# Optimization experiments

Measured on AMD Instinct MI355X. Metric: run time of the kernel, lower is better.

Reference implementation:

```python
import jax, jax.numpy as jnp
import numpy as np

EPS = 1e-5

def _ln(x, g, b):
    m = jnp.mean(x, -1, keepdims=True)
    v = jnp.var(x, -1, keepdims=True)
    return (x - m) / jnp.sqrt(v + EPS) * g + b

def _rel_shift(x):
    # x: [B, qlen, klen, n_head] -- TransformerXL relative shift
    b, q, k, n = x.shape
    xp = jnp.pad(x, ((0, 0), (0, 0), (1, 0), (0, 0)))  # zero-pad along klen front
    xp = xp.reshape(b, k + 1, q, n)[:, 1:]
    return xp.reshape(b, q, k, n)

def setup_inputs() -> dict:
    key = jax.random.key(0)
    B, Q, D, N, DH, DI = 4, 1024, 1024, 16, 64, 4096
    ks = jax.random.split(key, 9)
    s = 0.02
    w = jax.random.normal(ks[0], (B, Q, D), jnp.float32)
    r = jax.random.normal(ks[1], (1, Q, D), jnp.float32)
    attention_mask = jnp.triu(jnp.ones((Q, Q), bool), k=1)  # 1 == masked (causal)
    qkv_w = jax.random.normal(ks[2], (3 * D, D), jnp.float32) * s
    r_w = jax.random.normal(ks[3], (D, D), jnp.float32) * s
    o_w = jax.random.normal(ks[4], (D, D), jnp.float32) * s
    r_w_bias = jax.random.normal(ks[5], (N, DH), jnp.float32) * s
    r_r_bias = jax.random.normal(ks[6], (N, DH), jnp.float32) * s
    ln1_g = jnp.ones(D, jnp.float32); ln1_b = jnp.zeros(D, jnp.float32)
    ff_w1 = jax.random.normal(ks[7], (DI, D), jnp.float32) * s
    ff_b1 = jnp.zeros(DI, jnp.float32)
    ff_w2 = jax.random.normal(ks[8], (D, DI), jnp.float32) * s
    ff_b2 = jnp.zeros(D, jnp.float32)
    ln2_g = jnp.ones(D, jnp.float32); ln2_b = jnp.zeros(D, jnp.float32)
    return dict(w=w, r=r, attention_mask=attention_mask, qkv_w=qkv_w, r_w=r_w,
                o_w=o_w, r_w_bias=r_w_bias, r_r_bias=r_r_bias, ln1_g=ln1_g,
                ln1_b=ln1_b, ff_w1=ff_w1, ff_b1=ff_b1, ff_w2=ff_w2, ff_b2=ff_b2,
                ln2_g=ln2_g, ln2_b=ln2_b)

def reference(w, r, attention_mask, qkv_w, r_w, o_w, r_w_bias, r_r_bias,
              ln1_g, ln1_b, ff_w1, ff_b1, ff_w2, ff_b2, ln2_g, ln2_b):
    B, Q, D = w.shape
    N, DH = r_w_bias.shape
    # QKV projection (post-lnorm path, no mem)
    heads = w @ qkv_w.T  # [B,Q,3D]
    q, k, v = jnp.split(heads, 3, axis=-1)
    q = q.reshape(B, Q, N, DH)
    k = k.reshape(B, Q, N, DH)
    v = v.reshape(B, Q, N, DH)
    rk = (r[0] @ r_w.T).reshape(Q, N, DH)  # [rlen,N,DH]
    # content (AC) and position (BD) terms, computed in fp32 as in original
    AC = jnp.einsum('bind,bjnd->bijn', q + r_w_bias, k)
    BD = _rel_shift(jnp.einsum('bind,jnd->bijn', q + r_r_bias, rk))
    score = (AC + BD) * (1.0 / jnp.sqrt(jnp.float32(DH)))
    score = jnp.where(attention_mask[None, :, :, None], -1e30, score)
    prob = jax.nn.softmax(score, axis=2)  # softmax over klen
    av = jnp.einsum('bijn,bjnd->bind', prob, v).reshape(B, Q, D)
    out1 = _ln(w + av @ o_w.T, ln1_g, ln1_b)  # deepnorm_alpha = 1.0
    ff = jax.nn.relu(out1 @ ff_w1.T + ff_b1) @ ff_w2.T + ff_b2
    return _ln(out1 + ff, ln2_g, ln2_b)
```

## Files before the change

kernel.cpp:

```cpp
#include <hip/hip_runtime.h>
#include <hip/hip_bf16.h>

typedef __attribute__((ext_vector_type(8))) short short8;
typedef __attribute__((ext_vector_type(4))) short short4v;
typedef __attribute__((ext_vector_type(4))) float floatx4;

__device__ inline float bs2f(short s) {
    unsigned int u = ((unsigned int)(unsigned short)s) << 16;
    float f; __builtin_memcpy(&f, &u, 4); return f;
}
__device__ inline short f2bs(float f) {
    __hip_bfloat16 h = __float2bfloat16(f);
    unsigned short u; __builtin_memcpy(&u, &h, 2); return (short)u;
}
__device__ inline float ldf(const float* p)           { return *p; }
__device__ inline float ldf(const __hip_bfloat16* p)  { return __bfloat162float(*p); }
__device__ inline void  stf(float* p, float v)          { *p = v; }
__device__ inline void  stf(__hip_bfloat16* p, float v) { *p = __float2bfloat16(v); }

__device__ inline void gl_lds16(const short* g, short* l) {
    __builtin_amdgcn_global_load_lds(
        (const __attribute__((address_space(1))) void*)g,
        (__attribute__((address_space(3))) void*)l, 16, 0, 0);
}

__global__ __launch_bounds__(256) void f2b_all_kernel(
    const float* __restrict__ s0, const float* __restrict__ s1,
    const float* __restrict__ s2, const float* __restrict__ s3,
    const float* __restrict__ s4, const float* __restrict__ s5,
    const float* __restrict__ s6, __hip_bfloat16* __restrict__ dst)
{
    const long id  = blockIdx.x;
    const long gid = id * 1024 + threadIdx.x * 4;
    const float* src; long base;
    if      (id < 4096)  { src = s0; base = 0; }
    else if (id < 5120)  { src = s1; base = 4096L  * 1024; }
    else if (id < 8192)  { src = s2; base = 5120L  * 1024; }
    else if (id < 9216)  { src = s3; base = 8192L  * 1024; }
    else if (id < 10240) { src = s4; base = 9216L  * 1024; }
    else if (id < 14336) { src = s5; base = 10240L * 1024; }
    else                 { src = s6; base = 14336L * 1024; }
    const float4 v = *(const float4*)(src + (gid - base));
    dst[gid + 0] = __float2bfloat16(v.x);
    dst[gid + 1] = __float2bfloat16(v.y);
    dst[gid + 2] = __float2bfloat16(v.z);
    dst[gid + 3] = __float2bfloat16(v.w);
}

__global__ __launch_bounds__(256, 2) void gemm128_nt_kernel(
    const __hip_bfloat16* __restrict__ A,
    const __hip_bfloat16* __restrict__ Bw,
    __hip_bfloat16* __restrict__ C,
    int M, int N, int K,
    const float* __restrict__ bias,
    int do_relu)
{
    __shared__ short lA[128 * 32];
    __shared__ short lB[128 * 32];

    const int lane = threadIdx.x & 63;
    const int w    = threadIdx.x >> 6;
    const int m16  = lane & 15;
    const int quad = lane >> 4;
    const int wr   = w >> 1, wc = w & 1;

    const long i0 = (long)blockIdx.y * 128;
    const long j0 = (long)blockIdx.x * 128;

    const short* Ap = (const short*)A;
    const short* Bp = (const short*)Bw;

    floatx4 acc[4][4];
    #pragma unroll
    for (int a = 0; a < 4; ++a)
        #pragma unroll
        for (int b = 0; b < 4; ++b) acc[a][b] = (floatx4){0.f, 0.f, 0.f, 0.f};

    const int srow = w * 32 + (lane >> 2);
    const int scol = (lane & 3) * 8;
    const short* ga = Ap + (i0 + srow) * K + scol;
    const short* gb = Bp + (j0 + srow) * K + scol;
    short* la = lA + (w * 32) * 32;
    short* lb = lB + (w * 32) * 32;

    for (int k0 = 0; k0 < K; k0 += 32) {
        __syncthreads();
        gl_lds16(ga + k0,            la);
        gl_lds16(ga + 16 * K + k0,   la + 16 * 32);
        gl_lds16(gb + k0,            lb);
        gl_lds16(gb + 16 * K + k0,   lb + 16 * 32);
        __syncthreads();

        short8 af[4], bf[4];
        #pragma unroll
        for (int rb = 0; rb < 4; ++rb)
            af[rb] = *(const short8*)&lA[(wr * 64 + rb * 16 + m16) * 32 + quad * 8];
        #pragma unroll
        for (int cb = 0; cb < 4; ++cb)
            bf[cb] = *(const short8*)&lB[(wc * 64 + cb * 16 + m16) * 32 + quad * 8];
        #pragma unroll
        for (int rb = 0; rb < 4; ++rb)
            #pragma unroll
            for (int cb = 0; cb < 4; ++cb)
                acc[rb][cb] = __builtin_amdgcn_mfma_f32_16x16x32_bf16(
                    af[rb], bf[cb], acc[rb][cb], 0, 0, 0);
    }

    #pragma unroll
    for (int cb = 0; cb < 4; ++cb) {
        const long j = j0 + wc * 64 + cb * 16 + m16;
        const float bv = bias ? bias[j] : 0.f;
        #pragma unroll
        for (int rb = 0; rb < 4; ++rb) {
            #pragma unroll
            for (int rr = 0; rr < 4; ++rr) {
                const long row = i0 + wr * 64 + rb * 16 + quad * 4 + rr;
                float v = acc[rb][cb][rr] + bv;
                if (do_relu) v = fmaxf(v, 0.f);
                C[row * N + j] = __float2bfloat16(v);
            }
        }
    }
}

__global__ __launch_bounds__(256, 2) void gemm128_splitk_kernel(
    const __hip_bfloat16* __restrict__ A,
    const __hip_bfloat16* __restrict__ Bw,
    __hip_bfloat16* __restrict__ C0,
    __hip_bfloat16* __restrict__ C1,
    int M, int N, int K)
{
    __shared__ short lA[128 * 32];
    __shared__ short lB[128 * 32];

    const int lane = threadIdx.x & 63;
    const int w    = threadIdx.x >> 6;
    const int m16  = lane & 15;
    const int quad = lane >> 4;
    const int wr   = w >> 1, wc = w & 1;

    const long i0 = (long)blockIdx.y * 128;
    const long j0 = (long)blockIdx.x * 128;
    const int  kz = blockIdx.z;
    const int  kbeg = kz * (K >> 1), kend = kbeg + (K >> 1);

    const short* Ap = (const short*)A;
    const short* Bp = (const short*)Bw;

    floatx4 acc[4][4];
    #pragma unroll
    for (int a = 0; a < 4; ++a)
        #pragma unroll
        for (int b = 0; b < 4; ++b) acc[a][b] = (floatx4){0.f, 0.f, 0.f, 0.f};

    const int srow = w * 32 + (lane >> 2);
    const int scol = (lane & 3) * 8;
    const short* ga = Ap + (i0 + srow) * K + scol;
    const short* gb = Bp + (j0 + srow) * K + scol;
    short* la = lA + (w * 32) * 32;
    short* lb = lB + (w * 32) * 32;

    for (int k0 = kbeg; k0 < kend; k0 += 32) {
        __syncthreads();
        gl_lds16(ga + k0,            la);
        gl_lds16(ga + 16 * K + k0,   la + 16 * 32);
        gl_lds16(gb + k0,            lb);
        gl_lds16(gb + 16 * K + k0,   lb + 16 * 32);
        __syncthreads();

        short8 af[4], bf[4];
        #pragma unroll
        for (int rb = 0; rb < 4; ++rb)
            af[rb] = *(const short8*)&lA[(wr * 64 + rb * 16 + m16) * 32 + quad * 8];
        #pragma unroll
        for (int cb = 0; cb < 4; ++cb)
            bf[cb] = *(const short8*)&lB[(wc * 64 + cb * 16 + m16) * 32 + quad * 8];
        #pragma unroll
        for (int rb = 0; rb < 4; ++rb)
            #pragma unroll
            for (int cb = 0; cb < 4; ++cb)
                acc[rb][cb] = __builtin_amdgcn_mfma_f32_16x16x32_bf16(
                    af[rb], bf[cb], acc[rb][cb], 0, 0, 0);
    }

    __hip_bfloat16* C = kz ? C1 : C0;
    #pragma unroll
    for (int cb = 0; cb < 4; ++cb) {
        const long j = j0 + wc * 64 + cb * 16 + m16;
        #pragma unroll
        for (int rb = 0; rb < 4; ++rb) {
            #pragma unroll
            for (int rr = 0; rr < 4; ++rr) {
                const long row = i0 + wr * 64 + rb * 16 + quad * 4 + rr;
                C[row * N + j] = __float2bfloat16(acc[rb][cb][rr]);
            }
        }
    }
}

__global__ __launch_bounds__(256, 2) void gemm_n64_nt_kernel(
    const __hip_bfloat16* __restrict__ A,
    const __hip_bfloat16* __restrict__ Bw,
    __hip_bfloat16* __restrict__ C,
    int M, int N, int K,
    const float* __restrict__ bias,
    int do_relu)
{
    __shared__ short lA[128 * 32];
    __shared__ short lB[64 * 32];

    const int lane = threadIdx.x & 63;
    const int w    = threadIdx.x >> 6;
    const int m16  = lane & 15;
    const int quad = lane >> 4;
    const int wr   = w >> 1, wc = w & 1;

    const long i0 = (long)blockIdx.y * 128;
    const long j0 = (long)blockIdx.x * 64;

    const short* Ap = (const short*)A;
    const short* Bp = (const short*)Bw;

    floatx4 acc[4][2];
    #pragma unroll
    for (int a = 0; a < 4; ++a)
        #pragma unroll
        for (int b = 0; b < 2; ++b) acc[a][b] = (floatx4){0.f, 0.f, 0.f, 0.f};

    const int srowA = w * 32 + (lane >> 2);
    const int srowB = w * 16 + (lane >> 2);
    const int scol  = (lane & 3) * 8;
    const short* ga = Ap + (i0 + srowA) * K + scol;
    const short* gb = Bp + (j0 + srowB) * K + scol;
    short* la = lA + (w * 32) * 32;
    short* lb = lB + (w * 16) * 32;

    for (int k0 = 0; k0 < K; k0 += 32) {
        __syncthreads();
        gl_lds16(ga + k0,            la);
        gl_lds16(ga + 16 * K + k0,   la + 16 * 32);
        gl_lds16(gb + k0,            lb);
        __syncthreads();

        short8 af[4], bf[2];
        #pragma unroll
        for (int rb = 0; rb < 4; ++rb)
            af[rb] = *(const short8*)&lA[(wr * 64 + rb * 16 + m16) * 32 + quad * 8];
        #pragma unroll
        for (int cb = 0; cb < 2; ++cb)
            bf[cb] = *(const short8*)&lB[(wc * 32 + cb * 16 + m16) * 32 + quad * 8];
        #pragma unroll
        for (int rb = 0; rb < 4; ++rb)
            #pragma unroll
            for (int cb = 0; cb < 2; ++cb)
                acc[rb][cb] = __builtin_amdgcn_mfma_f32_16x16x32_bf16(
                    af[rb], bf[cb], acc[rb][cb], 0, 0, 0);
    }

    #pragma unroll
    for (int cb = 0; cb < 2; ++cb) {
        const long j = j0 + wc * 32 + cb * 16 + m16;
        const float bv = bias ? bias[j] : 0.f;
        #pragma unroll
        for (int rb = 0; rb < 4; ++rb) {
            #pragma unroll
            for (int rr = 0; rr < 4; ++rr) {
                const long row = i0 + wr * 64 + rb * 16 + quad * 4 + rr;
                float v = acc[rb][cb][rr] + bv;
                if (do_relu) v = fmaxf(v, 0.f);
                C[row * N + j] = __float2bfloat16(v);
            }
        }
    }
}

__global__ __launch_bounds__(256) void kvpack_kernel(
    const __hip_bfloat16* __restrict__ heads,
    short* __restrict__ kp, short* __restrict__ vp)
{
    const int Q = 1024, TD = 3072;
    __shared__ short kt[64 * 72];
    __shared__ short vt[64 * 72];
    const int tid = threadIdx.x;
    const int t  = blockIdx.x;
    const int bn = blockIdx.y;
    const int n = bn & 15, b = bn >> 4;
    const int j0 = t * 64;

    const short* hp = (const short*)heads + ((long)(b * Q + j0)) * TD + n * 64;
    {
        const int r = tid >> 2, c0 = (tid & 3) * 16;
        const short* src = hp + (long)r * TD + c0;
        *(short8*)&kt[r * 72 + c0]     = *(const short8*)(src + 1024);
        *(short8*)&kt[r * 72 + c0 + 8] = *(const short8*)(src + 1024 + 8);
        *(short8*)&vt[r * 72 + c0]     = *(const short8*)(src + 2048);
        *(short8*)&vt[r * 72 + c0 + 8] = *(const short8*)(src + 2048 + 8);
    }
    __syncthreads();

    const int lane = tid & 63;
    const int m16 = lane & 15, quad = lane >> 4;
    const long fb = ((long)bn * 16 + t) * 4096;
    #pragma unroll
    for (int pass = 0; pass < 2; ++pass) {
        const int fi = (tid >> 6) + pass * 4;
        const int c = fi >> 2, cb = fi & 3;
        short8 kf = *(const short8*)&kt[(cb * 16 + m16) * 72 + c * 32 + quad * 8];
        *(short8*)(kp + fb + fi * 512 + lane * 8) = kf;
        short8 vf;
        #pragma unroll
        for (int u = 0; u < 8; ++u)
            vf[u] = vt[(c * 32 + quad * 8 + u) * 72 + cb * 16 + m16];
        *(short8*)(vp + fb + fi * 512 + lane * 8) = vf;
    }
}

__global__ __launch_bounds__(256) void rkpack_kernel(
    const __hip_bfloat16* __restrict__ rkb, short* __restrict__ rkp)
{
    const int m = blockIdx.x;
    const int tid = threadIdx.x;
    const short4v v = *(const short4v*)((const short*)rkb + m * 1024 + tid * 4);
    const int n = tid >> 4, d = (tid * 4) & 63;
    *(short4v*)(rkp + ((long)n * 1024 + m) * 64 + d) = v;
}

__global__ __launch_bounds__(256, 2) void fattn_kernel(
    const __hip_bfloat16* __restrict__ heads,
    const short* __restrict__ kp,
    const short* __restrict__ vp,
    const short* __restrict__ rkp,
    const float* __restrict__ rwb,
    const float* __restrict__ rrb,
    __hip_bfloat16* __restrict__ av)
{
    const int Q = 1024, TD = 3072, D = 1024;
    const int tid  = threadIdx.x;
    const int lane = tid & 63;
    const int w    = tid >> 6;
    const int m16  = lane & 15;
    const int quad = lane >> 4;
    const int id = blockIdx.x;
    const int r8 = id & 7;
    const int z  = (id >> 3) & 7;
    const int bn = ((id >> 6) << 3) | r8;
    const int n = bn & 15, b = bn >> 4;

    __shared__ short pbuf[4][16 * 68];
    short* pb = pbuf[w];

    const short* hp = (const short*)heads;

    struct KV { short8 k[8], v[8]; };

    #pragma unroll
    for (int phase = 0; phase < 2; ++phase) {
        const int qt  = phase ? (15 - z) : z;
        const int iw0 = qt * 64 + w * 16;

        short8 qwf[2], qrf[2];
        {
            const long qoff = ((long)(b * Q + iw0 + m16)) * TD + n * 64;
            #pragma unroll
            for (int c = 0; c < 2; ++c) {
                short8 qv = *(const short8*)(hp + qoff + c * 32 + quad * 8);
                #pragma unroll
                for (int u = 0; u < 8; ++u) {
                    const int d = c * 32 + quad * 8 + u;
                    const float f = bs2f(qv[u]);
                    qwf[c][u] = f2bs(f + rwb[n * 64 + d]);
                    qrf[c][u] = f2bs(f + rrb[n * 64 + d]);
                }
            }
        }

        floatx4 oacc[4];
        #pragma unroll
        for (int t = 0; t < 4; ++t) oacc[t] = (floatx4){0.f, 0.f, 0.f, 0.f};
        float lsum[4] = {0.f, 0.f, 0.f, 0.f};

        auto loadKV = [&](KV& f, int t) {
            const long fb = ((long)bn * 16 + t) * 4096 + lane * 8;
            #pragma unroll
            for (int fi = 0; fi < 8; ++fi) {
                f.k[fi] = *(const short8*)(kp + fb + fi * 512);
                f.v[fi] = *(const short8*)(vp + fb + fi * 512);
            }
        };

        auto computeT = [&](const KV& f, int t) {
            const int j0 = t * 64;

            short8 rf[5][2];
            const int m0 = Q - 16 + j0 - iw0;
            #pragma unroll
            for (int cb = 0; cb < 5; ++cb) {
                int m = m0 + cb * 16 + m16;
                if (m > Q - 1) m = Q - 1;
                const long roff = ((long)n * 1024 + m) * 64;
                #pragma unroll
                for (int c = 0; c < 2; ++c)
                    rf[cb][c] = *(const short8*)(rkp + roff + c * 32 + quad * 8);
            }

            floatx4 ac[4];
            #pragma unroll
            for (int cb = 0; cb < 4; ++cb) ac[cb] = (floatx4){0.f, 0.f, 0.f, 0.f};
            #pragma unroll
            for (int c = 0; c < 2; ++c)
                #pragma unroll
                for (int cb = 0; cb < 4; ++cb)
                    ac[cb] = __builtin_amdgcn_mfma_f32_16x16x32_bf16(
                        qwf[c], f.k[c * 4 + cb], ac[cb], 0, 0, 0);

            floatx4 bd[5];
            #pragma unroll
            for (int cb = 0; cb < 5; ++cb) bd[cb] = (floatx4){0.f, 0.f, 0.f, 0.f};
            #pragma unroll
            for (int cb = 0; cb < 5; ++cb)
                #pragma unroll
                for (int c = 0; c < 2; ++c)
                    bd[cb] = __builtin_amdgcn_mfma_f32_16x16x32_bf16(
                        qrf[c], rf[cb][c], bd[cb], 0, 0, 0);

            #pragma unroll
            for (int r = 0; r < 4; ++r) {
                const int ii = quad * 4 + r;
                const int e  = 15 + m16 - ii;
                const int srcLane = (lane & 48) | (e & 15);
                float sh[5];
                #pragma unroll
                for (int cb = 0; cb < 5; ++cb)
                    sh[cb] = __shfl(bd[cb][r], srcLane, 64);
                #pragma unroll
                for (int cb = 0; cb < 4; ++cb) {
                    const float val = (e >= 16) ? sh[cb + 1] : sh[cb];
                    const float sc = (ac[cb][r] + val) * 0.125f;
                    const bool masked = (j0 + cb * 16 + m16) > (iw0 + ii);
                    const float p = masked ? 0.f : __expf(sc);
                    lsum[r] += p;
                    pb[ii * 68 + cb * 16 + m16] = f2bs(p);
                }
            }

            #pragma unroll
            for (int c = 0; c < 2; ++c) {
                const short* pp = pb + m16 * 68 + c * 32 + quad * 8;
                short4v plo = *(const short4v*)pp;
                short4v phi = *(const short4v*)(pp + 4);
                short8 pf;
                #pragma unroll
                for (int u = 0; u < 4; ++u) { pf[u] = plo[u]; pf[u + 4] = phi[u]; }
                #pragma unroll
                for (int cb = 0; cb < 4; ++cb)
                    oacc[cb] = __builtin_amdgcn_mfma_f32_16x16x32_bf16(
                        pf, f.v[c * 4 + cb], oacc[cb], 0, 0, 0);
            }
        };

        KV fa, fb;
        loadKV(fa, 0);
        int t = 0;
        for (;;) {
            if (t < qt) loadKV(fb, t + 1);
            computeT(fa, t);
            if (++t > qt) break;
            if (t < qt) loadKV(fa, t + 1);
            computeT(fb, t);
            if (++t > qt) break;
        }

        #pragma unroll
        for (int r = 0; r < 4; ++r) {
            #pragma unroll
            for (int sft = 1; sft < 16; sft <<= 1)
                lsum[r] += __shfl_xor(lsum[r], sft, 64);
        }
        #pragma unroll
        for (int r = 0; r < 4; ++r) {
            const float linv = 1.f / lsum[r];
            #pragma unroll
            for (int cb = 0; cb < 4; ++cb) {
                const long row = (long)b * Q + iw0 + quad * 4 + r;
                av[row * D + n * 64 + cb * 16 + m16] =
                    __float2bfloat16(oacc[cb][r] * linv);
            }
        }
    }
}

template <typename TA, typename TB, typename TO>
__global__ __launch_bounds__(256) void ln_kernel(
    const TA* __restrict__ xa,
    const TB* __restrict__ xb,
    const float* __restrict__ g,
    const float* __restrict__ beta,
    TO* __restrict__ out)
{
    const int D = 1024;
    const long row = blockIdx.x;
    const int tid = threadIdx.x;
    const TA* pa = xa + row * D;
    const TB* pb = xb + row * D;

    float x[4];
    float s = 0.f, s2 = 0.f;
    #pragma unroll
    for (int u = 0; u < 4; ++u) {
        const int c = tid + u * 256;
        const float v = ldf(pa + c) + ldf(pb + c);
        x[u] = v; s += v; s2 += v * v;
    }
    #pragma unroll
    for (int sft = 32; sft > 0; sft >>= 1) {
        s  += __shfl_xor(s,  sft, 64);
        s2 += __shfl_xor(s2, sft, 64);
    }
    __shared__ float red[8];
    const int wv = tid >> 6, lane = tid & 63;
    if (lane == 0) { red[wv] = s; red[wv + 4] = s2; }
    __syncthreads();
    s  = red[0] + red[1] + red[2] + red[3];
    s2 = red[4] + red[5] + red[6] + red[7];
    const float mean = s * (1.f / D);
    const float var  = s2 * (1.f / D) - mean * mean;
    const float rstd = rsqrtf(var + 1e-5f);
    #pragma unroll
    for (int u = 0; u < 4; ++u) {
        const int c = tid + u * 256;
        const float v = (x[u] - mean) * rstd * g[c] + beta[c];
        stf(out + row * D + c, v);
    }
}

template <typename TA, typename TO>
__global__ __launch_bounds__(256) void ln3_kernel(
    const TA* __restrict__ xa,
    const __hip_bfloat16* __restrict__ p0,
    const __hip_bfloat16* __restrict__ p1,
    const float* __restrict__ bias,
    const float* __restrict__ g,
    const float* __restrict__ beta,
    TO* __restrict__ out)
{
    const int D = 1024;
    const long row = blockIdx.x;
    const int tid = threadIdx.x;
    const TA* pa = xa + row * D;
    const __hip_bfloat16* q0 = p0 + row * D;
    const __hip_bfloat16* q1 = p1 + row * D;

    float x[4];
    float s = 0.f, s2 = 0.f;
    #pragma unroll
    for (int u = 0; u < 4; ++u) {
        const int c = tid + u * 256;
        float v = ldf(pa + c) + ldf(q0 + c) + ldf(q1 + c);
        if (bias) v += bias[c];
        x[u] = v; s += v; s2 += v * v;
    }
    #pragma unroll
    for (int sft = 32; sft > 0; sft >>= 1) {
        s  += __shfl_xor(s,  sft, 64);
        s2 += __shfl_xor(s2, sft, 64);
    }
    __shared__ float red[8];
    const int wv = tid >> 6, lane = tid & 63;
    if (lane == 0) { red[wv] = s; red[wv + 4] = s2; }
    __syncthreads();
    s  = red[0] + red[1] + red[2] + red[3];
    s2 = red[4] + red[5] + red[6] + red[7];
    const float mean = s * (1.f / D);
    const float var  = s2 * (1.f / D) - mean * mean;
    const float rstd = rsqrtf(var + 1e-5f);
    #pragma unroll
    for (int u = 0; u < 4; ++u) {
        const int c = tid + u * 256;
        const float v = (x[u] - mean) * rstd * g[c] + beta[c];
        stf(out + row * D + c, v);
    }
}

extern "C" void kernel_launch(void* const* d_in, const int* in_sizes, int n_in,
                              void* d_out, int out_size, void* d_ws, size_t ws_size,
                              hipStream_t stream)
{
    const int B = 4, Q = 1024, D = 1024, N = 16, TD = 3072, DI = 4096;
    const int BQ = B * Q;

    const float* w     = (const float*)d_in[0];
    const float* r     = (const float*)d_in[1];
    const float* qkv_w = (const float*)d_in[3];
    const float* r_w   = (const float*)d_in[4];
    const float* o_w   = (const float*)d_in[5];
    const float* rwb   = (const float*)d_in[6];
    const float* rrb   = (const float*)d_in[7];
    const float* ln1g  = (const float*)d_in[8];
    const float* ln1b  = (const float*)d_in[9];
    const float* ffw1  = (const float*)d_in[10];
    const float* ffb1  = (const float*)d_in[11];
    const float* ffw2  = (const float*)d_in[12];
    const float* ffb2  = (const float*)d_in[13];
    const float* ln2g  = (const float*)d_in[14];
    const float* ln2b  = (const float*)d_in[15];
    float* out = (float*)d_out;

    __hip_bfloat16* wsb   = (__hip_bfloat16*)d_ws;
    __hip_bfloat16* heads = wsb;
    __hip_bfloat16* rkb   = heads + (long)BQ * TD;
    __hip_bfloat16* av    = rkb   + (long)Q * D;
    __hip_bfloat16* ffh   = wsb;
    __hip_bfloat16* oproj = av    + (long)BQ * D;
    __hip_bfloat16* out1  = oproj + (long)BQ * D;
    __hip_bfloat16* cvt   = out1  + (long)BQ * D;
    __hip_bfloat16* wb    = cvt;
    __hip_bfloat16* rb    = wb    + (long)BQ * D;
    __hip_bfloat16* qkvwb = rb    + (long)Q * D;
    __hip_bfloat16* rwwb  = qkvwb + (long)TD * D;
    __hip_bfloat16* owb   = rwwb  + (long)D * D;
    __hip_bfloat16* f1wb  = owb   + (long)D * D;
    __hip_bfloat16* f2wb  = f1wb  + (long)DI * D;
    short* kp  = (short*)wb;
    short* vpk = (short*)rb;
    short* rkp = (short*)rwwb;
    __hip_bfloat16* part0 = wb;
    __hip_bfloat16* part1 = wb + (long)BQ * D;

    const dim3 blk(256);

    f2b_all_kernel<<<dim3(18432), blk, 0, stream>>>(
        w, r, qkv_w, r_w, o_w, ffw1, ffw2, wb);

    gemm128_nt_kernel<<<dim3(TD / 128, BQ / 128), blk, 0, stream>>>(
        wb, qkvwb, heads, BQ, TD, D, nullptr, 0);
    gemm_n64_nt_kernel<<<dim3(D / 64, Q / 128), blk, 0, stream>>>(
        rb, rwwb, rkb, Q, D, D, nullptr, 0);
    kvpack_kernel<<<dim3(16, B * N), blk, 0, stream>>>(heads, kp, vpk);
    rkpack_kernel<<<dim3(Q), blk, 0, stream>>>(rkb, rkp);
    fattn_kernel<<<dim3(512), blk, 0, stream>>>(
        heads, kp, vpk, rkp, rwb, rrb, av);
    gemm128_splitk_kernel<<<dim3(D / 128, BQ / 128, 2), blk, 0, stream>>>(
        av, owb, part0, part1, BQ, D, D);
    ln3_kernel<float, __hip_bfloat16>
        <<<dim3(BQ), blk, 0, stream>>>(w, part0, part1, nullptr, ln1g, ln1b, out1);
    gemm128_nt_kernel<<<dim3(DI / 128, BQ / 128), blk, 0, stream>>>(
        out1, f1wb, ffh, BQ, DI, D, ffb1, 1);
    gemm128_splitk_kernel<<<dim3(D / 128, BQ / 128, 2), blk, 0, stream>>>(
        ffh, f2wb, part0, part1, BQ, D, DI);
    ln3_kernel<__hip_bfloat16, float>
        <<<dim3(BQ), blk, 0, stream>>>(out1, part0, part1, ffb2, ln2g, ln2b, out);
}
```

Before: 395.7 us.

## Split attention KV range across wave pairs and merge kvpack/rkpack launches

```diff
diff --git a/kernel.cpp b/kernel.cpp
--- a/kernel.cpp
+++ b/kernel.cpp
@@ -274,14 +274,22 @@
     }
 }
 
-__global__ __launch_bounds__(256) void kvpack_kernel(
+__global__ __launch_bounds__(256) void pack_kernel(
     const __hip_bfloat16* __restrict__ heads,
-    short* __restrict__ kp, short* __restrict__ vp)
+    const __hip_bfloat16* __restrict__ rkb,
+    short* __restrict__ kp, short* __restrict__ vp, short* __restrict__ rkp)
 {
     const int Q = 1024, TD = 3072;
+    const int tid = threadIdx.x;
+    if (blockIdx.x >= 16) {
+        const int m = (blockIdx.x - 16) * 64 + blockIdx.y;
+        const short4v v = *(const short4v*)((const short*)rkb + m * 1024 + tid * 4);
+        const int n = tid >> 4, d = (tid * 4) & 63;
+        *(short4v*)(rkp + ((long)n * 1024 + m) * 64 + d) = v;
+        return;
+    }
     __shared__ short kt[64 * 72];
     __shared__ short vt[64 * 72];
-    const int tid = threadIdx.x;
     const int t  = blockIdx.x;
     const int bn = blockIdx.y;
     const int n = bn & 15, b = bn >> 4;
@@ -315,16 +323,6 @@
     }
 }
 
-__global__ __launch_bounds__(256) void rkpack_kernel(
-    const __hip_bfloat16* __restrict__ rkb, short* __restrict__ rkp)
-{
-    const int m = blockIdx.x;
-    const int tid = threadIdx.x;
-    const short4v v = *(const short4v*)((const short*)rkb + m * 1024 + tid * 4);
-    const int n = tid >> 4, d = (tid * 4) & 63;
-    *(short4v*)(rkp + ((long)n * 1024 + m) * 64 + d) = v;
-}
-
 __global__ __launch_bounds__(256, 2) void fattn_kernel(
     const __hip_bfloat16* __restrict__ heads,
     const short* __restrict__ kp,
@@ -342,194 +340,185 @@
     const int quad = lane >> 4;
     const int id = blockIdx.x;
     const int r8 = id & 7;
-    const int z  = (id >> 3) & 7;
-    const int bn = ((id >> 6) << 3) | r8;
+    const int s  = id >> 3;
+    const int cz = s & 31;
+    const int bn = ((s >> 5) << 3) | r8;
     const int n = bn & 15, b = bn >> 4;
 
+    const int c   = (w < 2) ? cz : (63 - cz);
+    const int h   = w & 1;
+    const int iw0 = c * 16;
+    const int T   = (c >> 2) + 1;
+    const int mid = T >> 1;
+    const int t0  = h ? mid : 0;
+    const int t1  = h ? T : mid;
+    const int slot = w >> 1;
+
     __shared__ short pbuf[4][16 * 68];
+    __shared__ float ocomb[2][16 * 68];
+    __shared__ float lcomb[2][16];
     short* pb = pbuf[w];
 
     const short* hp = (const short*)heads;
 
     struct KV { short8 k[8], v[8]; };
 
-    #pragma unroll
-    for (int phase = 0; phase < 2; ++phase) {
-        const int qt  = phase ? (15 - z) : z;
-        const int iw0 = qt * 64 + w * 16;
-
-        short8 qwf[2], qrf[2];
-        {
-            const long qoff = ((long)(b * Q + iw0 + m16)) * TD + n * 64;
-            #pragma unroll
-            for (int c = 0; c < 2; ++c) {
-                short8 qv = *(const short8*)(hp + qoff + c * 32 + quad * 8);
-                #pragma unroll
-                for (int u = 0; u < 8; ++u) {
-                    const int d = c * 32 + quad * 8 + u;
-                    const float f = bs2f(qv[u]);
-                    qwf[c][u] = f2bs(f + rwb[n * 64 + d]);
-                    qrf[c][u] = f2bs(f + rrb[n * 64 + d]);
-                }
+    short8 qwf[2], qrf[2];
+    {
+        const long qoff = ((long)(b * Q + iw0 + m16)) * TD + n * 64;
+        #pragma unroll
+        for (int cc = 0; cc < 2; ++cc) {
+            short8 qv = *(const short8*)(hp + qoff + cc * 32 + quad * 8);
+            #pragma unroll
+            for (int u = 0; u < 8; ++u) {
+                const int d = cc * 32 + quad * 8 + u;
+                const float f = bs2f(qv[u]);
+                qwf[cc][u] = f2bs(f + rwb[n * 64 + d]);
+                qrf[cc][u] = f2bs(f + rrb[n * 64 + d]);
             }
         }
-
-        floatx4 oacc[4];
-        #pragma unroll
-        for (int t = 0; t < 4; ++t) oacc[t] = (floatx4){0.f, 0.f, 0.f, 0.f};
-        float lsum[4] = {0.f, 0.f, 0.f, 0.f};
-
-        auto loadKV = [&](KV& f, int t) {
-            const long fb = ((long)bn * 16 + t) * 4096 + lane * 8;
-            #pragma unroll
-            for (int fi = 0; fi < 8; ++fi) {
-                f.k[fi] = *(const short8*)(kp + fb + fi * 512);
-                f.v[fi] = *(const short8*)(vp + fb + fi * 512);
+    }
+
+    floatx4 oacc[4];
+    #pragma unroll
+    for (int t = 0; t < 4; ++t) oacc[t] = (floatx4){0.f, 0.f, 0.f, 0.f};
+    float lsum[4] = {0.f, 0.f, 0.f, 0.f};
+
+    auto loadKV = [&](KV& f, int t) {
+        const long fb = ((long)bn * 16 + t) * 4096 + lane * 8;
+        #pragma unroll
+        for (int fi = 0; fi < 8; ++fi) {
+            f.k[fi] = *(const short8*)(kp + fb + fi * 512);
+            f.v[fi] = *(const short8*)(vp + fb + fi * 512);
+        }
+    };
+
+    auto computeT = [&](const KV& f, int t) {
+        const int j0 = t * 64;
+
+        short8 rf[5][2];
+        const int m0 = Q - 16 + j0 - iw0;
+        #pragma unroll
+        for (int cb = 0; cb < 5; ++cb) {
+            int m = m0 + cb * 16 + m16;
+            if (m > Q - 1) m = Q - 1;
+            const long roff = ((long)n * 1024 + m) * 64;
+            #pragma unroll
+            for (int cc = 0; cc < 2; ++cc)
+                rf[cb][cc] = *(const short8*)(rkp + roff + cc * 32 + quad * 8);
+        }
+
+        floatx4 ac[4];
+        #pragma unroll
+        for (int cb = 0; cb < 4; ++cb) ac[cb] = (floatx4){0.f, 0.f, 0.f, 0.f};
+        #pragma unroll
+        for (int cc = 0; cc < 2; ++cc)
+            #pragma unroll
+            for (int cb = 0; cb < 4; ++cb)
+                ac[cb] = __builtin_amdgcn_mfma_f32_16x16x32_bf16(
+                    qwf[cc], f.k[cc * 4 + cb], ac[cb], 0, 0, 0);
+
+        floatx4 bd[5];
+        #pragma unroll
+        for (int cb = 0; cb < 5; ++cb) bd[cb] = (floatx4){0.f, 0.f, 0.f, 0.f};
+        #pragma unroll
+        for (int cb = 0; cb < 5; ++cb)
+            #pragma unroll
+            for (int cc = 0; cc < 2; ++cc)
+                bd[cb] = __builtin_amdgcn_mfma_f32_16x16x32_bf16(
+                    qrf[cc], rf[cb][cc], bd[cb], 0, 0, 0);
+
+        #pragma unroll
+        for (int r = 0; r < 4; ++r) {
+            const int ii = quad * 4 + r;
+            const int e  = 15 + m16 - ii;
+            const int srcLane = (lane & 48) | (e & 15);
+            float sh[5];
+            #pragma unroll
+            for (int cb = 0; cb < 5; ++cb)
+                sh[cb] = __shfl(bd[cb][r], srcLane, 64);
+            #pragma unroll
+            for (int cb = 0; cb < 4; ++cb) {
+                const float val = (e >= 16) ? sh[cb + 1] : sh[cb];
+                const float sc = (ac[cb][r] + val) * 0.125f;
+                const bool masked = (j0 + cb * 16 + m16) > (iw0 + ii);
+                const float p = masked ? 0.f : __expf(sc);
+                lsum[r] += p;
+                pb[ii * 68 + cb * 16 + m16] = f2bs(p);
             }
-        };
-
-        auto computeT = [&](const KV& f, int t) {
-            const int j0 = t * 64;
-
-            short8 rf[5][2];
-            const int m0 = Q - 16 + j0 - iw0;
-            #pragma unroll
-            for (int cb = 0; cb < 5; ++cb) {
-                int m = m0 + cb * 16 + m16;
-                if (m > Q - 1) m = Q - 1;
-                const long roff = ((long)n * 1024 + m) * 64;
-                #pragma unroll
-                for (int c = 0; c < 2; ++c)
-                    rf[cb][c] = *(const short8*)(rkp + roff + c * 32 + quad * 8);
+        }
+
+        #pragma unroll
+        for (int cc = 0; cc < 2; ++cc) {
+            const short* pp = pb + m16 * 68 + cc * 32 + quad * 8;
+            short4v plo = *(const short4v*)pp;
+            short4v phi = *(const short4v*)(pp + 4);
+            short8 pf;
+            #pragma unroll
+            for (int u = 0; u < 4; ++u) { pf[u] = plo[u]; pf[u + 4] = phi[u]; }
+            #pragma unroll
+            for (int cb = 0; cb < 4; ++cb)
+                oacc[cb] = __builtin_amdgcn_mfma_f32_16x16x32_bf16(
+                    pf, f.v[cc * 4 + cb], oacc[cb], 0, 0, 0);
+        }
+    };
+
+    if (t0 < t1) {
+        KV fa, fb;
+        loadKV(fa, t0);
+        int t = t0;
+        for (;;) {
+            if (t + 1 < t1) loadKV(fb, t + 1);
+            computeT(fa, t);
+            if (++t >= t1) break;
+            if (t + 1 < t1) loadKV(fa, t + 1);
+            computeT(fb, t);
+            if (++t >= t1) break;
+        }
+    }
+
+    #pragma unroll
+    for (int r = 0; r < 4; ++r) {
+        #pragma unroll
+        for (int sft = 1; sft < 16; sft <<= 1)
+            lsum[r] += __shfl_xor(lsum[r], sft, 64);
+    }
+
+    if (h == 1) {
+        #pragma unroll
+        for (int r = 0; r < 4; ++r) {
+            const int ii = quad * 4 + r;
+            #pragma unroll
+            for (int cb = 0; cb < 4; ++cb)
+                ocomb[slot][ii * 68 + cb * 16 + m16] = oacc[cb][r];
+            if (m16 == 0) lcomb[slot][ii] = lsum[r];
+        }
+    }
+    __syncthreads();
+    if (h == 0) {
+        #pragma unroll
+        for (int r = 0; r < 4; ++r) {
+            const int ii = quad * 4 + r;
+            const float lt = lsum[r] + lcomb[slot][ii];
+            const float linv = 1.f / lt;
+            #pragma unroll
+            for (int cb = 0; cb < 4; ++cb) {
+                const float o = oacc[cb][r] + ocomb[slot][ii * 68 + cb * 16 + m16];
+                pb[ii * 64 + cb * 16 + m16] = f2bs(o * linv);
             }
-
-            floatx4 ac[4];
-            #pragma unroll
-            for (int cb = 0; cb < 4; ++cb) ac[cb] = (floatx4){0.f, 0.f, 0.f, 0.f};
-            #pragma unroll
-            for (int c = 0; c < 2; ++c)
-                #pragma unroll
-                for (int cb = 0; cb < 4; ++cb)
-                    ac[cb] = __builtin_amdgcn_mfma_f32_16x16x32_bf16(
-                        qwf[c], f.k[c * 4 + cb], ac[cb], 0, 0, 0);
-
-            floatx4 bd[5];
-            #pragma unroll
-            for (int cb = 0; cb < 5; ++cb) bd[cb] = (floatx4){0.f, 0.f, 0.f, 0.f};
-            #pragma unroll
-            for (int cb = 0; cb < 5; ++cb)
-                #pragma unroll
-                for (int c = 0; c < 2; ++c)
-                    bd[cb] = __builtin_amdgcn_mfma_f32_16x16x32_bf16(
-                        qrf[c], rf[cb][c], bd[cb], 0, 0, 0);
-
-            #pragma unroll
-            for (int r = 0; r < 4; ++r) {
-                const int ii = quad * 4 + r;
-                const int e  = 15 + m16 - ii;
-                const int srcLane = (lane & 48) | (e & 15);
-                float sh[5];
-                #pragma unroll
-                for (int cb = 0; cb < 5; ++cb)
-                    sh[cb] = __shfl(bd[cb][r], srcLane, 64);
-                #pragma unroll
-                for (int cb = 0; cb < 4; ++cb) {
-                    const float val = (e >= 16) ? sh[cb + 1] : sh[cb];
-                    const float sc = (ac[cb][r] + val) * 0.125f;
-                    const bool masked = (j0 + cb * 16 + m16) > (iw0 + ii);
-                    const float p = masked ? 0.f : __expf(sc);
-                    lsum[r] += p;
-                    pb[ii * 68 + cb * 16 + m16] = f2bs(p);
-                }
-            }
-
-            #pragma unroll
-            for (int c = 0; c < 2; ++c) {
-                const short* pp = pb + m16 * 68 + c * 32 + quad * 8;
-                short4v plo = *(const short4v*)pp;
-                short4v phi = *(const short4v*)(pp + 4);
-                short8 pf;
-                #pragma unroll
-                for (int u = 0; u < 4; ++u) { pf[u] = plo[u]; pf[u + 4] = phi[u]; }
-                #pragma unroll
-                for (int cb = 0; cb < 4; ++cb)
-                    oacc[cb] = __builtin_amdgcn_mfma_f32_16x16x32_bf16(
-                        pf, f.v[c * 4 + cb], oacc[cb], 0, 0, 0);
-            }
-        };
-
-        KV fa, fb;
-        loadKV(fa, 0);
-        int t = 0;
-        for (;;) {
-            if (t < qt) loadKV(fb, t + 1);
-            computeT(fa, t);
-            if (++t > qt) break;
-            if (t < qt) loadKV(fa, t + 1);
-            computeT(fb, t);
-            if (++t > qt) break;
-        }
-
-        #pragma unroll
-        for (int r = 0; r < 4; ++r) {
-            #pragma unroll
-            for (int sft = 1; sft < 16; sft <<= 1)
-                lsum[r] += __shfl_xor(lsum[r], sft, 64);
-        }
-        #pragma unroll
-        for (int r = 0; r < 4; ++r) {
-            const float linv = 1.f / lsum[r];
-            #pragma unroll
-            for (int cb = 0; cb < 4; ++cb) {
-                const long row = (long)b * Q + iw0 + quad * 4 + r;
-                av[row * D + n * 64 + cb * 16 + m16] =
-                    __float2bfloat16(oacc[cb][r] * linv);
-            }
-        }
-    }
-}
-
-template <typename TA, typename TB, typename TO>
-__global__ __launch_bounds__(256) void ln_kernel(
-    const TA* __restrict__ xa,
-    const TB* __restrict__ xb,
-    const float* __restrict__ g,
-    const float* __restrict__ beta,
-    TO* __restrict__ out)
-{
-    const int D = 1024;
-    const long row = blockIdx.x;
-    const int tid = threadIdx.x;
-    const TA* pa = xa + row * D;
-    const TB* pb = xb + row * D;
-
-    float x[4];
-    float s = 0.f, s2 = 0.f;
-    #pragma unroll
-    for (int u = 0; u < 4; ++u) {
-        const int c = tid + u * 256;
-        const float v = ldf(pa + c) + ldf(pb + c);
-        x[u] = v; s += v; s2 += v * v;
-    }
-    #pragma unroll
-    for (int sft = 32; sft > 0; sft >>= 1) {
-        s  += __shfl_xor(s,  sft, 64);
-        s2 += __shfl_xor(s2, sft, 64);
-    }
-    __shared__ float red[8];
-    const int wv = tid >> 6, lane = tid & 63;
-    if (lane == 0) { red[wv] = s; red[wv + 4] = s2; }
+        }
+    }
     __syncthreads();
-    s  = red[0] + red[1] + red[2] + red[3];
-    s2 = red[4] + red[5] + red[6] + red[7];
-    const float mean = s * (1.f / D);
-    const float var  = s2 * (1.f / D) - mean * mean;
-    const float rstd = rsqrtf(var + 1e-5f);
-    #pragma unroll
-    for (int u = 0; u < 4; ++u) {
-        const int c = tid + u * 256;
-        const float v = (x[u] - mean) * rstd * g[c] + beta[c];
-        stf(out + row * D + c, v);
+    if (h == 0) {
+        short* avp = (short*)av;
+        const long rowbase = (long)b * Q + iw0;
+        #pragma unroll
+        for (int u = 0; u < 2; ++u) {
+            const int rr = u * 8 + (lane >> 3);
+            const int cc = (lane & 7) * 8;
+            short8 o = *(const short8*)&pb[rr * 64 + cc];
+            *(short8*)(avp + (rowbase + rr) * D + n * 64 + cc) = o;
+        }
     }
 }
 
@@ -635,9 +624,8 @@
         wb, qkvwb, heads, BQ, TD, D, nullptr, 0);
     gemm_n64_nt_kernel<<<dim3(D / 64, Q / 128), blk, 0, stream>>>(
         rb, rwwb, rkb, Q, D, D, nullptr, 0);
-    kvpack_kernel<<<dim3(16, B * N), blk, 0, stream>>>(heads, kp, vpk);
-    rkpack_kernel<<<dim3(Q), blk, 0, stream>>>(rkb, rkp);
-    fattn_kernel<<<dim3(512), blk, 0, stream>>>(
+    pack_kernel<<<dim3(32, B * N), blk, 0, stream>>>(heads, rkb, kp, vpk, rkp);
+    fattn_kernel<<<dim3(2048), blk, 0, stream>>>(
         heads, kp, vpk, rkp, rwb, rrb, av);
     gemm128_splitk_kernel<<<dim3(D / 128, BQ / 128, 2), blk, 0, stream>>>(
         av, owb, part0, part1, BQ, D, D);
```

After: 397.6 us. No clear change (+0.5%).
